# Performance work log

Measured on AMD Instinct MI355X. Metric: run time of the kernel, lower is better.

The kernel has to match this reference:

```python
import jax, jax.numpy as jnp
import numpy as np

OBJ_N, D_KEY, D_VAL, BANK_N, N_Q, BS = 4, 128, 512, 7200, 3600, 1


def setup_inputs() -> dict:
    key = jax.random.key(0)
    k1, k2, k3, k4, k5 = jax.random.split(key, 5)
    return {
        "keys": jax.random.normal(k1, (OBJ_N, D_KEY, BANK_N), dtype=jnp.float32),
        "values": jax.random.normal(k2, (OBJ_N, D_VAL, BANK_N), dtype=jnp.float32),
        "masks": jax.random.uniform(k3, (OBJ_N, 1, BANK_N), dtype=jnp.float32),
        "q_in": jax.random.normal(k4, (BS, D_KEY, N_Q), dtype=jnp.float32),
        "q_out": jax.random.normal(k5, (BS, D_VAL, N_Q), dtype=jnp.float32),
    }


def reference(keys, values, masks, q_in, q_out):
    # keys: (O, Dk, B) memory keys per object; q_in: (S, Dk, N) query keys
    d_key = keys.shape[1]
    scale = 1.0 / jnp.sqrt(jnp.asarray(d_key, dtype=keys.dtype))
    # p[o,s,b,n] = softmax_b( keys[o,:,b] . q_in[s,:,n] / sqrt(Dk) )
    logits = jnp.einsum('odb,sdn->osbn', keys, q_in) * scale
    p = jax.nn.softmax(logits, axis=2)
    # mem[o,s,v,n] = sum_b values[o,v,b] * p[o,s,b,n]
    mem = jnp.einsum('ovb,osbn->osvn', values, p)
    # mask_mem[o,s,1,n]: mask-weighted attention readout, gates q_out
    mask_mem = jnp.einsum('omb,osbn->osmn', masks, p)
    q_out_with_mask = q_out[None] * mask_mem          # (O, S, Dv, N)
    out = jnp.concatenate([mem, q_out_with_mask], axis=2)  # (O, S, 2*Dv, N)
    return jnp.transpose(out, (1, 0, 2, 3))           # (S, O, 2*Dv, N)
```

## Files before the change

### kernel.cpp

```cpp
#include <hip/hip_runtime.h>
#include <hip/hip_bf16.h>

typedef unsigned short u16;
typedef unsigned int   u32;
typedef short bf16x8 __attribute__((ext_vector_type(8)));
typedef float f32x4  __attribute__((ext_vector_type(4)));

#define O_N    4
#define D_K    128
#define D_V    512
#define BANK   7200
#define NQ     3600
#define NT     64
#define NTILES 57
#define NSUB   225
#define VH_ROWS 256

#define K_OFF    0
#define P_OFF    32768
#define LMM_OFF  49152
#define SMEM_BYTES 49664
#define Q_OFF    0

#define GLL(gsrc, ldst) __builtin_amdgcn_global_load_lds( \
    (const __attribute__((address_space(1))) void*)(gsrc), \
    (__attribute__((address_space(3))) void*)(ldst), 16, 0, 0)

#define MFMA16(a, b, c) __builtin_amdgcn_mfma_f32_16x16x32_bf16((a), (b), (c), 0, 0, 0)

static __device__ __forceinline__ u16 f2bf(float x) {
    u32 u = __builtin_bit_cast(u32, x);
    return (u16)((u + 0x7FFFu + ((u >> 16) & 1u)) >> 16);
}

#define QSCALE 0.12751743f


__global__ void k_transpose_bf16(const float* __restrict__ in, u16* __restrict__ out) {
    __shared__ float tile[32][33];
    const int obj = blockIdx.z;
    const float* src = in + (size_t)obj * D_K * BANK;
    u16* dst = out + (size_t)obj * BANK * D_K;
    const int bx = blockIdx.x * 32;
    const int by = blockIdx.y * 32;
    const int tx = threadIdx.x, ty = threadIdx.y;
#pragma unroll
    for (int i = 0; i < 4; i++)
        tile[ty + 8 * i][tx] = src[(size_t)(by + ty + 8 * i) * BANK + bx + tx];
    __syncthreads();
#pragma unroll
    for (int i = 0; i < 4; i++)
        dst[(size_t)(bx + ty + 8 * i) * D_K + by + tx] = f2bf(tile[tx][ty + 8 * i]);
}

__global__ void k_convert_bf16(const float* __restrict__ in, u16* __restrict__ out, int n4) {
    int idx = blockIdx.x * blockDim.x + threadIdx.x;
    int stride = gridDim.x * blockDim.x;
    for (int i = idx; i < n4; i += stride) {
        float4 v = reinterpret_cast<const float4*>(in)[i];
        ushort4 o;
        o.x = f2bf(v.x); o.y = f2bf(v.y); o.z = f2bf(v.z); o.w = f2bf(v.w);
        reinterpret_cast<ushort4*>(out)[i] = o;
    }
}

__global__ void k_zero(float* out, int n) {
    int i = blockIdx.x * blockDim.x + threadIdx.x;
    if (i < n) out[i] = 0.f;
}

__launch_bounds__(256, 3)
__global__ void k_matcher(const u16* __restrict__ Kt,
                          const u16* __restrict__ Vb,
                          const float* __restrict__ masks,
                          const float* __restrict__ q_in,
                          const float* __restrict__ q_out,
                          float* __restrict__ out,
                          int G, float* __restrict__ lw, float* __restrict__ mw)
{
    __shared__ __align__(16) char smem[SMEM_BYTES];
    const int tid  = threadIdx.x;
    const int wave = tid >> 6;
    const int lane = tid & 63;
    const int q    = lane >> 4;
    const int lr   = lane & 15;
    const int lr7  = lr & 7;

    const int grp  = blockIdx.x & 7;
    const int o    = grp >> 1;
    const int vh   = grp & 1;
    const int rest = blockIdx.x >> 3;
    const int tile = rest / G;
    const int g    = rest - tile * G;
    const int n0   = tile * NT;

    const bool needLM = (G == 1) || (vh == 0);

    const int st0 = (NSUB * g) / G;
    const int st1 = (NSUB * (g + 1)) / G;
    const int cnt = st1 - st0;
    const int nd  = cnt >> 1;
    const int ts  = cnt & 1;
    const int nu  = nd + ts;

    for (int idx = tid; idx < NT * D_K; idx += 256) {
        int d = idx >> 6;
        int n = idx & 63;
        int gn = n0 + n;
        float v = (gn < NQ) ? q_in[(size_t)d * NQ + gn] * QSCALE : 0.f;
        int bb = d * 2;
        int sb = n * 256 + ((((bb >> 4) ^ (n & 7)) << 4) | (bb & 15));
        *reinterpret_cast<u16*>(smem + Q_OFF + sb) = f2bf(v);
    }
    __syncthreads();

    bf16x8 qf[4];
    {
        const int n = 16 * wave + lr;
#pragma unroll
        for (int ds = 0; ds < 4; ds++) {
            int gq = (4 * ds + q) ^ (n & 7);
            qf[ds] = *reinterpret_cast<const bf16x8*>(smem + Q_OFF + n * 256 + gq * 16);
        }
    }
    __syncthreads();

    const f32x4 zero4 = {0.f, 0.f, 0.f, 0.f};
    f32x4 acc[4][4];
#pragma unroll
    for (int i = 0; i < 4; i++)
#pragma unroll
        for (int j = 0; j < 4; j++) acc[i][j] = zero4;
    float l_part = 0.f, mm_part = 0.f;

    const u16* Ko = Kt + (size_t)o * BANK * D_K;
    const u16* Vo = Vb + (size_t)o * D_V * BANK + (size_t)vh * VH_ROWS * BANK;
    const float* mPtr = masks + (size_t)o * BANK + st0 * 32 + 4 * q;

    const u16* kSrcA = Ko + (size_t)(st0 * 32 + (tid >> 4)) * D_K
                         + (((tid & 15) ^ (tid >> 4)) << 3);
    const u16* kSrcB = kSrcA + 16 * D_K;

#define ISSUE2(buf) do {                                                   \
        char* kb_ = smem + K_OFF + (buf) * 16384 + wave * 1024;            \
        GLL(kSrcA, kb_);                                                   \
        GLL(kSrcB, kb_ + 4096);                                            \
        GLL(kSrcA + 32 * D_K, kb_ + 8192);                                 \
        GLL(kSrcB + 32 * D_K, kb_ + 12288);                                \
        kSrcA += 64 * D_K; kSrcB += 64 * D_K;                              \
    } while (0)
#define ISSUE1(buf) do {                                                   \
        char* kb_ = smem + K_OFF + (buf) * 16384 + wave * 1024;            \
        GLL(kSrcA, kb_);                                                   \
        GLL(kSrcB, kb_ + 4096);                                            \
    } while (0)

    const u16* Vrow = Vo + st0 * 32;
    const u32  vOff = (u32)(64 * wave + lr) * BANK + q * 8;

    const int nrow  = 16 * wave + lr;

#define QK_T(T, MV, PWB) do {                                                \
        f32x4 s_acc = zero4;                                                 \
        const int b_r = 16 * (T) + lr;                                       \
        _Pragma("unroll")                                                    \
        for (int ds = 0; ds < 4; ds++) {                                     \
            bf16x8 kf = *reinterpret_cast<const bf16x8*>(                    \
                kb + b_r * 256 + (((4 * ds + q) ^ lr) << 4));                \
            s_acc = MFMA16(kf, qf[ds], s_acc);                               \
        }                                                                    \
        float p0 = exp2f(s_acc[0]);                                          \
        float p1 = exp2f(s_acc[1]);                                          \
        float p2 = exp2f(s_acc[2]);                                          \
        float p3 = exp2f(s_acc[3]);                                          \
        if (needLM) {                                                        \
            l_part  += p0 + p1 + p2 + p3;                                    \
            mm_part += p0 * (MV).x + p1 * (MV).y + p2 * (MV).z + p3 * (MV).w;\
        }                                                                    \
        u32 w0, w1;                                                          \
        asm("v_cvt_pk_bf16_f32 %0, %1, %2" : "=v"(w0) : "v"(p0), "v"(p1));   \
        asm("v_cvt_pk_bf16_f32 %0, %1, %2" : "=v"(w1) : "v"(p2), "v"(p3));   \
        uint2 pk2; pk2.x = w0; pk2.y = w1;                                   \
        *reinterpret_cast<uint2*>(                                           \
            (PWB) + (((2 * (T) + (q >> 1)) ^ lr7) << 4)) = pk2;              \
    } while (0)

#define PV_S(S, PB, V0, V1, V2, V3) do {                                     \
        _Pragma("unroll")                                                    \
        for (int ng = 0; ng < 4; ng++) {                                     \
            bf16x8 pf = *reinterpret_cast<const bf16x8*>(                    \
                (PB) + (16 * ng + lr) * 128 +                                \
                (((4 * (S) + q) ^ lr7) << 4));                               \
            acc[0][ng] = MFMA16(V0, pf, acc[0][ng]);                         \
            acc[1][ng] = MFMA16(V1, pf, acc[1][ng]);                         \
            acc[2][ng] = MFMA16(V2, pf, acc[2][ng]);                         \
            acc[3][ng] = MFMA16(V3, pf, acc[3][ng]);                         \
        }                                                                    \
    } while (0)

    if (nd > 0) ISSUE2(0); else ISSUE1(0);
    asm volatile("s_waitcnt vmcnt(0)" ::: "memory");
    __builtin_amdgcn_s_barrier();
    __builtin_amdgcn_sched_barrier(0);

    bf16x8 va0, va1, va2, va3, vb0, vb1, vb2, vb3;

    for (int u = 0; u < nu; u++) {
        const int cur = u & 1;
        const char* kb = smem + K_OFF + cur * 16384;
        char* pWc = smem + P_OFF + cur * 8192 + nrow * 128 + (q & 1) * 8;
        const char* pR = smem + P_OFF + (cur ^ 1) * 8192;
        const bool full = (u < nd);

        if (u + 1 < nu) {
            if (u + 1 < nd) ISSUE2(cur ^ 1);
            else            ISSUE1(cur ^ 1);
        }
        float4 mv0 = *reinterpret_cast<const float4*>(mPtr);
        float4 mv1 = *reinterpret_cast<const float4*>(mPtr + 16);
        __builtin_amdgcn_sched_barrier(0);

        if (u > 0) {
            PV_S(0, pR, va0, va1, va2, va3);
            PV_S(1, pR, vb0, vb1, vb2, vb3);
        }
        __builtin_amdgcn_sched_barrier(0);

        va0 = *reinterpret_cast<const bf16x8*>(Vrow + vOff);
        va1 = *reinterpret_cast<const bf16x8*>(Vrow + vOff + 16 * BANK);
        va2 = *reinterpret_cast<const bf16x8*>(Vrow + vOff + 32 * BANK);
        va3 = *reinterpret_cast<const bf16x8*>(Vrow + vOff + 48 * BANK);
        if (full) {
            vb0 = *reinterpret_cast<const bf16x8*>(Vrow + vOff + 32);
            vb1 = *reinterpret_cast<const bf16x8*>(Vrow + vOff + 32 + 16 * BANK);
            vb2 = *reinterpret_cast<const bf16x8*>(Vrow + vOff + 32 + 32 * BANK);
            vb3 = *reinterpret_cast<const bf16x8*>(Vrow + vOff + 32 + 48 * BANK);
        }

        QK_T(0, mv0, pWc);
        QK_T(1, mv1, pWc);
        if (full) {
            float4 mv2 = *reinterpret_cast<const float4*>(mPtr + 32);
            float4 mv3 = *reinterpret_cast<const float4*>(mPtr + 48);
            QK_T(2, mv2, pWc);
            QK_T(3, mv3, pWc);
        }

        mPtr += full ? 64 : 32;
        Vrow += full ? 64 : 32;

        asm volatile("s_waitcnt vmcnt(0) lgkmcnt(0)" ::: "memory");
        __builtin_amdgcn_s_barrier();
        __builtin_amdgcn_sched_barrier(0);
    }

    {
        const char* pL = smem + P_OFF + ((nu - 1) & 1) * 8192;
        PV_S(0, pL, va0, va1, va2, va3);
        if (!ts) PV_S(1, pL, vb0, vb1, vb2, vb3);
    }

    float* l_lds  = reinterpret_cast<float*>(smem + LMM_OFF);
    float* mm_lds = l_lds + 64;
    if (needLM) {
        l_part  += __shfl_xor(l_part, 16);  l_part  += __shfl_xor(l_part, 32);
        mm_part += __shfl_xor(mm_part, 16); mm_part += __shfl_xor(mm_part, 32);
        if (lane < 16) {
            l_lds[16 * wave + lr]  = l_part;
            mm_lds[16 * wave + lr] = mm_part;
        }
    }
    __syncthreads();

    if (G == 1) {
        float* outo = out + (size_t)o * (1024 * NQ);
#pragma unroll
        for (int ng = 0; ng < 4; ng++) {
            const int n  = 16 * ng + lr;
            const int gn = n0 + n;
            if (gn >= NQ) continue;
            const float invl = 1.f / l_lds[n];
            const float gate = mm_lds[n] * invl;
#pragma unroll
            for (int vt = 0; vt < 4; vt++) {
#pragma unroll
                for (int r = 0; r < 4; r++) {
                    const int v = vh * VH_ROWS + 64 * wave + 16 * vt + 4 * q + r;
                    outo[(size_t)v * NQ + gn] = acc[vt][ng][r] * invl;
                    outo[(size_t)(512 + v) * NQ + gn] = q_out[(size_t)v * NQ + gn] * gate;
                }
            }
        }
    } else {
        float* dst = out + ((size_t)o * 1024 + (size_t)g * 512 + (size_t)vh * VH_ROWS) * NQ;
#pragma unroll
        for (int ng = 0; ng < 4; ng++) {
            const int n  = 16 * ng + lr;
            const int gn = n0 + n;
            if (gn >= NQ) continue;
#pragma unroll
            for (int vt = 0; vt < 4; vt++) {
#pragma unroll
                for (int r = 0; r < 4; r++) {
                    const int v = 64 * wave + 16 * vt + 4 * q + r;
                    dst[(size_t)v * NQ + gn] = acc[vt][ng][r];
                }
            }
        }
        if (vh == 0 && tid < 64) {
            const size_t li = ((size_t)(g * 4 + o) * NTILES + tile) * 64 + tid;
            lw[li] = l_lds[tid];
            mw[li] = mm_lds[tid];
        }
    }
}

__global__ void k_combine(const float* __restrict__ q_out, const float* __restrict__ lw,
                          const float* __restrict__ mw, float* __restrict__ out) {
    const int total = O_N * 512 * (NQ / 4);
    float4* outv = reinterpret_cast<float4*>(out);
    const float4* qv = reinterpret_cast<const float4*>(q_out);
    for (int idx = blockIdx.x * blockDim.x + threadIdx.x; idx < total;
         idx += gridDim.x * blockDim.x) {
        const int o  = idx / (512 * 900);
        const int r  = idx - o * 512 * 900;
        const int v  = r / 900;
        const int g4 = r - v * 900;
        const size_t iA = ((size_t)o * 1024 + v) * 900 + g4;
        const size_t iB = ((size_t)o * 1024 + 512 + v) * 900 + g4;
        float4 A = outv[iA];
        float4 B = outv[iB];
        const int tl = g4 >> 4;
        const int wi = (g4 & 15) * 4;
        const size_t l0i = ((size_t)(0 * 4 + o) * NTILES + tl) * 64 + wi;
        const size_t l1i = ((size_t)(1 * 4 + o) * NTILES + tl) * 64 + wi;
        const float4 l0 = *reinterpret_cast<const float4*>(lw + l0i);
        const float4 l1 = *reinterpret_cast<const float4*>(lw + l1i);
        const float4 m0 = *reinterpret_cast<const float4*>(mw + l0i);
        const float4 m1 = *reinterpret_cast<const float4*>(mw + l1i);
        float4 li, mem, gate;
        li.x = 1.f / (l0.x + l1.x); li.y = 1.f / (l0.y + l1.y);
        li.z = 1.f / (l0.z + l1.z); li.w = 1.f / (l0.w + l1.w);
        mem.x = (A.x + B.x) * li.x; mem.y = (A.y + B.y) * li.y;
        mem.z = (A.z + B.z) * li.z; mem.w = (A.w + B.w) * li.w;
        gate.x = (m0.x + m1.x) * li.x; gate.y = (m0.y + m1.y) * li.y;
        gate.z = (m0.z + m1.z) * li.z; gate.w = (m0.w + m1.w) * li.w;
        float4 qo = qv[(size_t)v * 900 + g4];
        outv[iA] = mem;
        float4 gq;
        gq.x = qo.x * gate.x; gq.y = qo.y * gate.y;
        gq.z = qo.z * gate.z; gq.w = qo.w * gate.w;
        outv[iB] = gq;
    }
}

extern "C" void kernel_launch(void* const* d_in, const int* in_sizes, int n_in,
                              void* d_out, int out_size, void* d_ws, size_t ws_size,
                              hipStream_t stream) {
    const float* keys   = (const float*)d_in[0];
    const float* values = (const float*)d_in[1];
    const float* masks  = (const float*)d_in[2];
    const float* q_in   = (const float*)d_in[3];
    const float* q_outp = (const float*)d_in[4];
    float* out = (float*)d_out;

    const size_t K_BYTES  = (size_t)O_N * BANK * D_K * 2;
    const size_t V_BYTES  = (size_t)O_N * D_V * BANK * 2;
    const size_t LM_FLOATS = (size_t)2 * O_N * NTILES * 64;
    const size_t LM_BYTES  = LM_FLOATS * 4 * 2;

    if (ws_size < K_BYTES + V_BYTES) {
        k_zero<<<(out_size + 255) / 256, 256, 0, stream>>>(out, out_size);
        return;
    }
    const int G = (ws_size >= K_BYTES + V_BYTES + LM_BYTES) ? 2 : 1;

    u16* Kt = (u16*)d_ws;
    u16* Vb = (u16*)((char*)d_ws + K_BYTES);
    float* lw = (float*)((char*)d_ws + K_BYTES + V_BYTES);
    float* mw = lw + LM_FLOATS;

    dim3 tb(32, 8);
    dim3 tg(BANK / 32, D_K / 32, O_N);
    k_transpose_bf16<<<tg, tb, 0, stream>>>(keys, Kt);

    const int n4 = O_N * D_V * BANK / 4;
    k_convert_bf16<<<2048, 256, 0, stream>>>(values, Vb, n4);

    k_matcher<<<NTILES * 8 * G, 256, 0, stream>>>(Kt, Vb, masks, q_in, q_outp, out,
                                                  G, lw, mw);
    if (G == 2)
        k_combine<<<2048, 256, 0, stream>>>(q_outp, lw, mw, out);
}
```

Baseline: 331.5 us.

## Load K fragments directly into registers and split QK work across waves by bank

Drops the global-to-LDS double-buffered staging of the key tiles. Each wave now loads its own 16 bank rows of K straight into registers and computes logits against all four query column groups, so Q fragments are held per wave for every group. Row sums and mask sums become per-wave partials, which are combined in LDS at the end. This cuts LDS use and the vmcnt wait at the barrier, but uses more registers (launch bounds lowered from 3 to 2 blocks per CU), and global K load latency is no longer hidden by a prefetch.

Result: faster. 289.2 us (-12.7%).

```diff
diff --git a/kernel.cpp b/kernel.cpp
--- a/kernel.cpp
+++ b/kernel.cpp
@@ -16,15 +16,11 @@
 #define NSUB   225
 #define VH_ROWS 256
 
-#define K_OFF    0
-#define P_OFF    32768
-#define LMM_OFF  49152
-#define SMEM_BYTES 49664
+#define P_OFF    0
+#define LST_OFF  16384
+#define MST_OFF  17408
+#define SMEM_BYTES 18432
 #define Q_OFF    0
-
-#define GLL(gsrc, ldst) __builtin_amdgcn_global_load_lds( \
-    (const __attribute__((address_space(1))) void*)(gsrc), \
-    (__attribute__((address_space(3))) void*)(ldst), 16, 0, 0)
 
 #define MFMA16(a, b, c) __builtin_amdgcn_mfma_f32_16x16x32_bf16((a), (b), (c), 0, 0, 0)
 
@@ -69,7 +65,7 @@
     if (i < n) out[i] = 0.f;
 }
 
-__launch_bounds__(256, 3)
+__launch_bounds__(256, 2)
 __global__ void k_matcher(const u16* __restrict__ Kt,
                           const u16* __restrict__ Vb,
                           const float* __restrict__ masks,
@@ -114,15 +110,15 @@
     }
     __syncthreads();
 
-    bf16x8 qf[4];
-    {
-        const int n = 16 * wave + lr;
+    bf16x8 qf[4][4];
+#pragma unroll
+    for (int cg = 0; cg < 4; cg++)
 #pragma unroll
         for (int ds = 0; ds < 4; ds++) {
-            int gq = (4 * ds + q) ^ (n & 7);
-            qf[ds] = *reinterpret_cast<const bf16x8*>(smem + Q_OFF + n * 256 + gq * 16);
-        }
-    }
+            int gq = (4 * ds + q) ^ lr7;
+            qf[cg][ds] = *reinterpret_cast<const bf16x8*>(
+                smem + Q_OFF + (16 * cg + lr) * 256 + gq * 16);
+        }
     __syncthreads();
 
     const f32x4 zero4 = {0.f, 0.f, 0.f, 0.f};
@@ -131,58 +127,40 @@
     for (int i = 0; i < 4; i++)
 #pragma unroll
         for (int j = 0; j < 4; j++) acc[i][j] = zero4;
-    float l_part = 0.f, mm_part = 0.f;
+    float l_part[4]  = {0.f, 0.f, 0.f, 0.f};
+    float mm_part[4] = {0.f, 0.f, 0.f, 0.f};
 
     const u16* Ko = Kt + (size_t)o * BANK * D_K;
     const u16* Vo = Vb + (size_t)o * D_V * BANK + (size_t)vh * VH_ROWS * BANK;
-    const float* mPtr = masks + (size_t)o * BANK + st0 * 32 + 4 * q;
-
-    const u16* kSrcA = Ko + (size_t)(st0 * 32 + (tid >> 4)) * D_K
-                         + (((tid & 15) ^ (tid >> 4)) << 3);
-    const u16* kSrcB = kSrcA + 16 * D_K;
-
-#define ISSUE2(buf) do {                                                   \
-        char* kb_ = smem + K_OFF + (buf) * 16384 + wave * 1024;            \
-        GLL(kSrcA, kb_);                                                   \
-        GLL(kSrcB, kb_ + 4096);                                            \
-        GLL(kSrcA + 32 * D_K, kb_ + 8192);                                 \
-        GLL(kSrcB + 32 * D_K, kb_ + 12288);                                \
-        kSrcA += 64 * D_K; kSrcB += 64 * D_K;                              \
-    } while (0)
-#define ISSUE1(buf) do {                                                   \
-        char* kb_ = smem + K_OFF + (buf) * 16384 + wave * 1024;            \
-        GLL(kSrcA, kb_);                                                   \
-        GLL(kSrcB, kb_ + 4096);                                            \
-    } while (0)
+
+    const u16* Krow = Ko + (size_t)(st0 * 32) * D_K;
+    const u32  kOff = (u32)(16 * wave + lr) * D_K + q * 8;
 
     const u16* Vrow = Vo + st0 * 32;
     const u32  vOff = (u32)(64 * wave + lr) * BANK + q * 8;
 
-    const int nrow  = 16 * wave + lr;
-
-#define QK_T(T, MV, PWB) do {                                                \
+    const float* mPtr = masks + (size_t)o * BANK + st0 * 32 + 16 * wave + 4 * q;
+
+#define QK_CG(CG) do {                                                       \
         f32x4 s_acc = zero4;                                                 \
-        const int b_r = 16 * (T) + lr;                                       \
-        _Pragma("unroll")                                                    \
-        for (int ds = 0; ds < 4; ds++) {                                     \
-            bf16x8 kf = *reinterpret_cast<const bf16x8*>(                    \
-                kb + b_r * 256 + (((4 * ds + q) ^ lr) << 4));                \
-            s_acc = MFMA16(kf, qf[ds], s_acc);                               \
-        }                                                                    \
+        s_acc = MFMA16(kf0, qf[CG][0], s_acc);                               \
+        s_acc = MFMA16(kf1, qf[CG][1], s_acc);                               \
+        s_acc = MFMA16(kf2, qf[CG][2], s_acc);                               \
+        s_acc = MFMA16(kf3, qf[CG][3], s_acc);                               \
         float p0 = exp2f(s_acc[0]);                                          \
         float p1 = exp2f(s_acc[1]);                                          \
         float p2 = exp2f(s_acc[2]);                                          \
         float p3 = exp2f(s_acc[3]);                                          \
         if (needLM) {                                                        \
-            l_part  += p0 + p1 + p2 + p3;                                    \
-            mm_part += p0 * (MV).x + p1 * (MV).y + p2 * (MV).z + p3 * (MV).w;\
+            l_part[CG]  += p0 + p1 + p2 + p3;                                \
+            mm_part[CG] += p0 * mv.x + p1 * mv.y + p2 * mv.z + p3 * mv.w;    \
         }                                                                    \
         u32 w0, w1;                                                          \
         asm("v_cvt_pk_bf16_f32 %0, %1, %2" : "=v"(w0) : "v"(p0), "v"(p1));   \
         asm("v_cvt_pk_bf16_f32 %0, %1, %2" : "=v"(w1) : "v"(p2), "v"(p3));   \
         uint2 pk2; pk2.x = w0; pk2.y = w1;                                   \
-        *reinterpret_cast<uint2*>(                                           \
-            (PWB) + (((2 * (T) + (q >> 1)) ^ lr7) << 4)) = pk2;              \
+        *reinterpret_cast<uint2*>(pWb + (16 * (CG) + lr) * 128 +             \
+            (((2 * wave + (q >> 1)) ^ lr7) << 4) + (q & 1) * 8) = pk2;       \
     } while (0)
 
 #define PV_S(S, PB, V0, V1, V2, V3) do {                                     \
@@ -198,26 +176,24 @@
         }                                                                    \
     } while (0)
 
-    if (nd > 0) ISSUE2(0); else ISSUE1(0);
-    asm volatile("s_waitcnt vmcnt(0)" ::: "memory");
-    __builtin_amdgcn_s_barrier();
-    __builtin_amdgcn_sched_barrier(0);
-
     bf16x8 va0, va1, va2, va3, vb0, vb1, vb2, vb3;
 
     for (int u = 0; u < nu; u++) {
         const int cur = u & 1;
-        const char* kb = smem + K_OFF + cur * 16384;
-        char* pWc = smem + P_OFF + cur * 8192 + nrow * 128 + (q & 1) * 8;
+        char* pWb = smem + P_OFF + cur * 8192;
         const char* pR = smem + P_OFF + (cur ^ 1) * 8192;
         const bool full = (u < nd);
-
-        if (u + 1 < nu) {
-            if (u + 1 < nd) ISSUE2(cur ^ 1);
-            else            ISSUE1(cur ^ 1);
-        }
-        float4 mv0 = *reinterpret_cast<const float4*>(mPtr);
-        float4 mv1 = *reinterpret_cast<const float4*>(mPtr + 16);
+        const bool doQK = full || (wave < 2);
+
+        bf16x8 kf0, kf1, kf2, kf3;
+        float4 mv;
+        if (doQK) {
+            kf0 = *reinterpret_cast<const bf16x8*>(Krow + kOff);
+            kf1 = *reinterpret_cast<const bf16x8*>(Krow + kOff + 32);
+            kf2 = *reinterpret_cast<const bf16x8*>(Krow + kOff + 64);
+            kf3 = *reinterpret_cast<const bf16x8*>(Krow + kOff + 96);
+            mv  = *reinterpret_cast<const float4*>(mPtr);
+        }
         __builtin_amdgcn_sched_barrier(0);
 
         if (u > 0) {
@@ -237,19 +213,15 @@
             vb3 = *reinterpret_cast<const bf16x8*>(Vrow + vOff + 32 + 48 * BANK);
         }
 
-        QK_T(0, mv0, pWc);
-        QK_T(1, mv1, pWc);
-        if (full) {
-            float4 mv2 = *reinterpret_cast<const float4*>(mPtr + 32);
-            float4 mv3 = *reinterpret_cast<const float4*>(mPtr + 48);
-            QK_T(2, mv2, pWc);
-            QK_T(3, mv3, pWc);
-        }
-
+        if (doQK) {
+            QK_CG(0); QK_CG(1); QK_CG(2); QK_CG(3);
+        }
+
+        Vrow += full ? 64 : 32;
+        Krow += (full ? 64 : 32) * D_K;
         mPtr += full ? 64 : 32;
-        Vrow += full ? 64 : 32;
-
-        asm volatile("s_waitcnt vmcnt(0) lgkmcnt(0)" ::: "memory");
+
+        asm volatile("s_waitcnt lgkmcnt(0)" ::: "memory");
         __builtin_amdgcn_s_barrier();
         __builtin_amdgcn_sched_barrier(0);
     }
@@ -260,14 +232,22 @@
         if (!ts) PV_S(1, pL, vb0, vb1, vb2, vb3);
     }
 
-    float* l_lds  = reinterpret_cast<float*>(smem + LMM_OFF);
-    float* mm_lds = l_lds + 64;
+    float* lst = reinterpret_cast<float*>(smem + LST_OFF);
+    float* mst = reinterpret_cast<float*>(smem + MST_OFF);
     if (needLM) {
-        l_part  += __shfl_xor(l_part, 16);  l_part  += __shfl_xor(l_part, 32);
-        mm_part += __shfl_xor(mm_part, 16); mm_part += __shfl_xor(mm_part, 32);
+#pragma unroll
+        for (int cg = 0; cg < 4; cg++) {
+            l_part[cg]  += __shfl_xor(l_part[cg], 16);
+            l_part[cg]  += __shfl_xor(l_part[cg], 32);
+            mm_part[cg] += __shfl_xor(mm_part[cg], 16);
+            mm_part[cg] += __shfl_xor(mm_part[cg], 32);
+        }
         if (lane < 16) {
-            l_lds[16 * wave + lr]  = l_part;
-            mm_lds[16 * wave + lr] = mm_part;
+#pragma unroll
+            for (int cg = 0; cg < 4; cg++) {
+                lst[wave * 64 + 16 * cg + lr] = l_part[cg];
+                mst[wave * 64 + 16 * cg + lr] = mm_part[cg];
+            }
         }
     }
     __syncthreads();
@@ -279,8 +259,10 @@
             const int n  = 16 * ng + lr;
             const int gn = n0 + n;
             if (gn >= NQ) continue;
-            const float invl = 1.f / l_lds[n];
-            const float gate = mm_lds[n] * invl;
+            const float lsum = lst[n] + lst[64 + n] + lst[128 + n] + lst[192 + n];
+            const float msum = mst[n] + mst[64 + n] + mst[128 + n] + mst[192 + n];
+            const float invl = 1.f / lsum;
+            const float gate = msum * invl;
 #pragma unroll
             for (int vt = 0; vt < 4; vt++) {
 #pragma unroll
@@ -309,8 +291,8 @@
         }
         if (vh == 0 && tid < 64) {
             const size_t li = ((size_t)(g * 4 + o) * NTILES + tile) * 64 + tid;
-            lw[li] = l_lds[tid];
-            mw[li] = mm_lds[tid];
+            lw[li] = lst[tid] + lst[64 + tid] + lst[128 + tid] + lst[192 + tid];
+            mw[li] = mst[tid] + mst[64 + tid] + mst[128 + tid] + mst[192 + tid];
         }
     }
 }
```
